# Kernel tuning notes

Measured on AMD Instinct MI355X. Metric: run time of the kernel, lower is better.

The kernel has to match this reference:

```python
import jax, jax.numpy as jnp
import numpy as np

B, N, DIM = 4, 1024, 1024
H, DH = 16, 64
NUM_MEM = 4
TOPK = 64
QK_SCALE = 10.0  # qk_norm_scale


def l2norm(t, eps=1e-12):
    # qk_norm_groups == 1 -> normalize over full head dim
    return t / jnp.clip(jnp.linalg.norm(t, axis=-1, keepdims=True), eps)


def setup_inputs() -> dict:
    key = jax.random.key(0)
    ks = jax.random.split(key, 12)
    s = 0.02
    inp = {
        "x": jax.random.normal(ks[0], (B, N, DIM), dtype=jnp.float32),
        "Wq": jax.random.normal(ks[1], (DIM, H * DH), dtype=jnp.float32) * s,
        "Wk": jax.random.normal(ks[2], (DIM, H * DH), dtype=jnp.float32) * s,
        "Wv": jax.random.normal(ks[3], (DIM, H * DH), dtype=jnp.float32) * s,
        "W_pre_th": jax.random.normal(ks[4], (H, H), dtype=jnp.float32) * (1.0 / H) ** 0.5,
        "W_post_th": jax.random.normal(ks[5], (H, H), dtype=jnp.float32) * (1.0 / H) ** 0.5,
        "mem_k": jax.random.normal(ks[6], (H, NUM_MEM, DH), dtype=jnp.float32),
        "mem_v": jax.random.normal(ks[7], (H, NUM_MEM, DH), dtype=jnp.float32),
        "head_scale_params": jnp.ones((1, H, 1, 1), dtype=jnp.float32),
        "Wg": jax.random.normal(ks[8], (DIM, H * DH), dtype=jnp.float32) * s,
        "bg": jnp.ones((H * DH,), dtype=jnp.float32),
        "Wo": jax.random.normal(ks[9], (H * DH, DIM), dtype=jnp.float32) * s,
    }
    return inp


def reference(x, Wq, Wk, Wv, W_pre_th, W_post_th, mem_k, mem_v,
              head_scale_params, Wg, bg, Wo):
    b, n, _ = x.shape
    # projections -> b h n d
    q = (x @ Wq).reshape(b, n, H, DH).transpose(0, 2, 1, 3)
    k = (x @ Wk).reshape(b, n, H, DH).transpose(0, 2, 1, 3)
    v = (x @ Wv).reshape(b, n, H, DH).transpose(0, 2, 1, 3)

    # memory key/values prepended along the key axis
    mk = jnp.broadcast_to(mem_k[None], (b, H, NUM_MEM, DH))
    mv = jnp.broadcast_to(mem_v[None], (b, H, NUM_MEM, DH))
    k = jnp.concatenate([mk, k], axis=2)
    v = jnp.concatenate([mv, v], axis=2)

    # qk-norm: l2 normalize then fixed scale
    q = l2norm(q)
    k = l2norm(k)

    dots = jnp.einsum("bhid,bhjd->bhij", q, k) * QK_SCALE  # b h n (n+m)
    # pre-softmax talking heads (1x1 conv over head channels)
    dots = jnp.einsum("hg,bgij->bhij", W_pre_th, dots)

    mask_value = -jnp.finfo(dots.dtype).max
    j = n + NUM_MEM
    # causal mask, left-padded False over the memory columns
    col_pos = jnp.arange(j) - NUM_MEM  # mem cols get negative pos -> never masked
    causal = jnp.arange(n)[:, None] < col_pos[None, :]  # (n, j)
    dots = jnp.where(causal[None, None], mask_value, dots)

    # sparse top-k: keep only entries >= k-th largest per row
    top = jax.lax.top_k(dots, TOPK)[0]
    vk = top[..., -1:]
    dots = jnp.where(dots < vk, mask_value, dots)

    attn = jax.nn.softmax(dots, axis=-1)
    # post-softmax talking heads
    attn = jnp.einsum("hg,bgij->bhij", W_post_th, attn)

    out = jnp.einsum("bhij,bhjd->bhid", attn, v)
    out = out * head_scale_params
    out = out.transpose(0, 2, 1, 3).reshape(b, n, H * DH)

    gates = x @ Wg + bg
    out = out * jax.nn.sigmoid(gates)
    return out @ Wo
```

## Files before the change

kernel.cpp:

```cpp
#include <hip/hip_runtime.h>
#include <hip/hip_bf16.h>
#include <float.h>

#define B_ 4
#define N_ 1024
#define H_ 16
#define DH_ 64
#define NM_ 4
#define J_ 1028
#define IT_ 4
#define TOPK_ 64
#define QKSCALE 10.0f
#define KTF_BG 67584
#define VTF_DC 16896

typedef __attribute__((ext_vector_type(8))) short short8;
typedef __attribute__((ext_vector_type(4))) float f32x4;
typedef __attribute__((ext_vector_type(8))) unsigned short ushort8;
typedef __attribute__((ext_vector_type(4))) unsigned int u32x4;
typedef __attribute__((ext_vector_type(2))) unsigned int u32x2;
typedef _Float16 half8 __attribute__((ext_vector_type(8)));

__device__ __forceinline__ unsigned short f2b(float f){
  union { float f; unsigned int i; } c; c.f = f;
  unsigned int r = c.i + 0x7FFFu + ((c.i >> 16) & 1u);
  return (unsigned short)(r >> 16);
}
__device__ __forceinline__ unsigned short f2h(float f){
  return __builtin_bit_cast(unsigned short, (_Float16)f);
}
__device__ __forceinline__ float h2f(unsigned short u){
  return (float)__builtin_bit_cast(_Float16, u);
}
__device__ __forceinline__ unsigned int h2key(unsigned int u){
  return (u & 0x8000u) ? (~u & 0xFFFFu) : (u | 0x8000u);
}
__device__ __forceinline__ float key2f(unsigned int k){
  unsigned int u = (k & 0x8000u) ? (k & 0x7FFFu) : (~k & 0xFFFFu);
  return h2f((unsigned short)u);
}

__global__ __launch_bounds__(256) void k_cvtAll(
    const float* __restrict__ x,  const float* __restrict__ wq,
    const float* __restrict__ wk, const float* __restrict__ wv,
    const float* __restrict__ wg, const float* __restrict__ wo,
    unsigned short* __restrict__ xb, unsigned short* __restrict__ wcatT,
    unsigned short* __restrict__ wobT,
    const float* __restrict__ mk, const float* __restrict__ mv,
    unsigned short* __restrict__ ktF, unsigned short* __restrict__ vtF){
  const int t = threadIdx.x;
  const unsigned bid = blockIdx.x;
  if (bid < 1280){
    __shared__ unsigned short tile[64][70];
    const int which = bid >> 8;
    const int tl = bid & 255;
    const int tr = tl >> 4, tc = tl & 15;
    const float* src = which == 0 ? wq : which == 1 ? wk : which == 2 ? wv : which == 3 ? wg : wo;
    {
      int r = t >> 2, c0 = (t & 3) * 16;
      const float* sp = src + (size_t)(tr * 64 + r) * 1024 + tc * 64 + c0;
      #pragma unroll
      for (int e = 0; e < 16; ++e) tile[r][c0 + e] = f2b(sp[e]);
    }
    __syncthreads();
    {
      int rn = t >> 2, k0 = (t & 3) * 16;
      int n = tc * 64 + rn;
      unsigned short* dp = (which == 4)
        ? wobT + (size_t)n * 1024 + tr * 64 + k0
        : wcatT + ((size_t)which * 1024 + n) * 1024 + tr * 64 + k0;
      ushort8 v0, v1;
      #pragma unroll
      for (int e = 0; e < 8; ++e) v0[e] = tile[k0 + e][rn];
      #pragma unroll
      for (int e = 0; e < 8; ++e) v1[e] = tile[k0 + 8 + e][rn];
      *(ushort8*)dp = v0;
      *(ushort8*)(dp + 8) = v1;
    }
    return;
  }
  if (bid >= 1280 && bid < 1284){
    int h = (bid - 1280) * 4 + (t >> 6);
    int d = t & 63;
    unsigned short kh[4], vh[4];
    #pragma unroll
    for (int mm = 0; mm < 4; ++mm){
      float kv = mk[(h * 4 + mm) * 64 + d];
      float ss = kv * kv;
      #pragma unroll
      for (int off = 32; off; off >>= 1) ss += __shfl_xor(ss, off);
      kh[mm] = f2h(kv / fmaxf(sqrtf(ss), 1e-12f));
      vh[mm] = f2h(mv[(h * 4 + mm) * 64 + d]);
    }
    for (int b = 0; b < B_; ++b){
      int bg = b * 16 + h;
      #pragma unroll
      for (int mm = 0; mm < 4; ++mm)
        ktF[(size_t)bg * KTF_BG + (size_t)(d >> 5) * 512 + (mm + ((d >> 3) & 3) * 16) * 8 + (d & 7)] = kh[mm];
      #pragma unroll
      for (int mm = 0; mm < 4; ++mm)
        vtF[(size_t)bg * KTF_BG + (size_t)(d >> 4) * VTF_DC + (d & 15) * 8 + mm] = vh[mm];
      {
        unsigned int* kz = (unsigned int*)(ktF + (size_t)bg * KTF_BG + 64 * 1024);
        for (int c = d; c < 1024; c += 64) kz[c] = 0u;
      }
      #pragma unroll
      for (int dc = 0; dc < 4; ++dc){
        unsigned int* vz = (unsigned int*)(vtF + (size_t)bg * KTF_BG + (size_t)dc * VTF_DC + 32 * 512);
        for (int c = d; c < 256; c += 64) vz[c] = 0u;
      }
    }
    return;
  }
  int i = (bid - 1284) * 256 + t;
  const int st = (3072 - 1284) * 256;
  for (; i < 4096 * 1024; i += st) xb[i] = f2b(x[i]);
}

__global__ __launch_bounds__(256) void k_gemmF(const unsigned short* __restrict__ A,
                                               const unsigned short* __restrict__ WcT,
                                               unsigned short* __restrict__ qn,
                                               unsigned short* __restrict__ ktF,
                                               unsigned short* __restrict__ vtF,
                                               unsigned short* __restrict__ gate,
                                               const float* __restrict__ bgv)
{
  __shared__ unsigned short As[128][72];
  __shared__ unsigned short Bs[64][72];
  const int t = threadIdx.x;
  const int m0 = blockIdx.y * 128, n0 = blockIdx.x * 64;
  const int l = t & 63, w = t >> 6;
  const int l15 = l & 15, l4 = l >> 4;

  f32x4 acc[2][4];
  #pragma unroll
  for (int a = 0; a < 2; ++a)
    #pragma unroll
    for (int b2 = 0; b2 < 4; ++b2) acc[a][b2] = (f32x4){0.f, 0.f, 0.f, 0.f};

  for (int k0 = 0; k0 < 1024; k0 += 64){
    #pragma unroll
    for (int cc = 0; cc < 4; ++cc){
      int c = t + cc * 256;
      int row = c >> 3, colc = (c & 7) * 8;
      *(ushort8*)&As[row][colc] = *(const ushort8*)&A[(m0 + row) * 1024 + k0 + colc];
    }
    #pragma unroll
    for (int cc = 0; cc < 2; ++cc){
      int c = t + cc * 256;
      int row = c >> 3, colc = (c & 7) * 8;
      *(ushort8*)&Bs[row][colc] = *(const ushort8*)&WcT[(size_t)(n0 + row) * 1024 + k0 + colc];
    }
    __syncthreads();
    #pragma unroll
    for (int ks = 0; ks < 64; ks += 32){
      short8 af[2], bfr[4];
      #pragma unroll
      for (int mf = 0; mf < 2; ++mf) af[mf]  = *(const short8*)&As[w * 32 + mf * 16 + l15][ks + l4 * 8];
      #pragma unroll
      for (int nf = 0; nf < 4; ++nf) bfr[nf] = *(const short8*)&Bs[nf * 16 + l15][ks + l4 * 8];
      #pragma unroll
      for (int mf = 0; mf < 2; ++mf)
        #pragma unroll
        for (int nf = 0; nf < 4; ++nf)
          acc[mf][nf] = __builtin_amdgcn_mfma_f32_16x16x32_bf16(af[mf], bfr[nf], acc[mf][nf], 0, 0, 0);
    }
    __syncthreads();
  }

  const int which = n0 >> 10;
  const int ncol0 = n0 & 1023;
  const int hcol = ncol0 >> 6;
  #pragma unroll
  for (int mf = 0; mf < 2; ++mf){
    if (which == 2){
      int row0 = m0 + w * 32 + mf * 16 + l4 * 4;
      int bb = row0 >> 10;
      int j0 = (row0 & 1023) + NM_;
      int jtE = j0 >> 5, lj = (j0 & 31) >> 3, e0 = j0 & 7;
      #pragma unroll
      for (int nf = 0; nf < 4; ++nf){
        int col = ncol0 + nf * 16 + l15;
        int h = col >> 6, d = col & 63;
        unsigned int lo = (unsigned int)f2h(acc[mf][nf][0]) | ((unsigned int)f2h(acc[mf][nf][1]) << 16);
        unsigned int hi = (unsigned int)f2h(acc[mf][nf][2]) | ((unsigned int)f2h(acc[mf][nf][3]) << 16);
        unsigned short* dst = vtF + (size_t)(bb * 16 + h) * KTF_BG +
                              (size_t)(d >> 4) * VTF_DC + (size_t)jtE * 512 +
                              ((d & 15) + lj * 16) * 8 + e0;
        *(u32x2*)dst = (u32x2){lo, hi};
      }
    } else {
      #pragma unroll
      for (int r = 0; r < 4; ++r){
        int row = m0 + w * 32 + mf * 16 + l4 * 4 + r;
        float rn = 1.f;
        if (which <= 1){
          float ss = 0.f;
          #pragma unroll
          for (int nf = 0; nf < 4; ++nf) ss += acc[mf][nf][r] * acc[mf][nf][r];
          #pragma unroll
          for (int off = 1; off < 16; off <<= 1) ss += __shfl_xor(ss, off);
          rn = 1.f / fmaxf(sqrtf(ss), 1e-12f);
          if (which == 0) rn *= QKSCALE;
        }
        #pragma unroll
        for (int nf = 0; nf < 4; ++nf){
          int col = ncol0 + nf * 16 + l15;
          float v = acc[mf][nf][r];
          int bb = row >> 10, ii = row & 1023;
          if (which == 3){
            float g = v + bgv[3 * 1024 + col];
            gate[(size_t)row * 1024 + col] = f2h(1.f / (1.f + __expf(-g)));
          } else if (which == 0){
            int d = col & 63;
            qn[((size_t)(bb * H_ + hcol) * N_ + ii) * DH_ + d] = f2h(v * rn);
          } else {
            int j = ii + NM_;
            int d = col & 63;
            ktF[(size_t)(bb * 16 + hcol) * KTF_BG + (size_t)(j >> 4) * 1024 +
                (size_t)(d >> 5) * 512 + ((j & 15) + ((d >> 3) & 3) * 16) * 8 + (d & 7)]
              = f2h(v * rn);
          }
        }
      }
    }
  }
}

__global__ __launch_bounds__(256) void k_gemmO(const unsigned short* __restrict__ A,
                                               const unsigned short* __restrict__ WT,
                                               float* __restrict__ outp)
{
  __shared__ unsigned short As[128][72];
  __shared__ unsigned short Bs[64][72];
  const int t = threadIdx.x;
  const int m0 = blockIdx.y * 128, n0 = blockIdx.x * 64;
  const int l = t & 63, w = t >> 6;
  const int l15 = l & 15, l4 = l >> 4;

  f32x4 acc[2][4];
  #pragma unroll
  for (int a = 0; a < 2; ++a)
    #pragma unroll
    for (int b2 = 0; b2 < 4; ++b2) acc[a][b2] = (f32x4){0.f, 0.f, 0.f, 0.f};

  for (int k0 = 0; k0 < 1024; k0 += 64){
    #pragma unroll
    for (int cc = 0; cc < 4; ++cc){
      int c = t + cc * 256;
      int row = c >> 3, colc = (c & 7) * 8;
      *(ushort8*)&As[row][colc] = *(const ushort8*)&A[(m0 + row) * 1024 + k0 + colc];
    }
    #pragma unroll
    for (int cc = 0; cc < 2; ++cc){
      int c = t + cc * 256;
      int row = c >> 3, colc = (c & 7) * 8;
      *(ushort8*)&Bs[row][colc] = *(const ushort8*)&WT[(size_t)(n0 + row) * 1024 + k0 + colc];
    }
    __syncthreads();
    #pragma unroll
    for (int ks = 0; ks < 64; ks += 32){
      short8 af[2], bfr[4];
      #pragma unroll
      for (int mf = 0; mf < 2; ++mf) af[mf]  = *(const short8*)&As[w * 32 + mf * 16 + l15][ks + l4 * 8];
      #pragma unroll
      for (int nf = 0; nf < 4; ++nf) bfr[nf] = *(const short8*)&Bs[nf * 16 + l15][ks + l4 * 8];
      #pragma unroll
      for (int mf = 0; mf < 2; ++mf)
        #pragma unroll
        for (int nf = 0; nf < 4; ++nf)
          acc[mf][nf] = __builtin_amdgcn_mfma_f32_16x16x32_bf16(af[mf], bfr[nf], acc[mf][nf], 0, 0, 0);
    }
    __syncthreads();
  }

  #pragma unroll
  for (int mf = 0; mf < 2; ++mf)
    #pragma unroll
    for (int r = 0; r < 4; ++r){
      int row = m0 + w * 32 + mf * 16 + l4 * 4 + r;
      #pragma unroll
      for (int nf = 0; nf < 4; ++nf)
        outp[(size_t)row * 1024 + n0 + nf * 16 + l15] = acc[mf][nf][r];
    }
}

template<int NJTE_MAX>
__global__ __launch_bounds__(1024) void k_attnM(
  const unsigned short* __restrict__ qn, const unsigned short* __restrict__ ktF,
  const unsigned short* __restrict__ vtF, const float* __restrict__ wpre,
  const float* __restrict__ wpost, const float* __restrict__ hsc,
  const unsigned short* __restrict__ gate, unsigned short* __restrict__ aout,
  int itBase)
{
  constexpr int JSTT = NJTE_MAX * 32 + 8;
  constexpr int NG = (JSTT + 127) / 128;
  __shared__ unsigned short sd[16 * IT_ * JSTT];
  __shared__ unsigned short qls[16 * 4 * 64];
  __shared__ unsigned short wpre16[16 * 32];
  __shared__ unsigned short wpost16[16 * 32];

  const int blk = blockIdx.x;
  const int b = (blk >> 1) & 3;
  const int idx = ((blk >> 3) << 1) | (blk & 1);
  const int it = itBase - idx;
  const int i0 = it * IT_;
  const int nAmax = i0 + IT_ + 4;
  const int nJtA = (nAmax + 15) >> 4;
  const int nJtE = (nAmax + 31) >> 5;
  const int nJtD = nJtE * 2;
  const int jc = nJtE * 32;
  const int t = threadIdx.x;
  const int w = t >> 6, l = t & 63;
  const int l15 = l & 15, l4 = l >> 4;

  if (t < 256){
    int h = t >> 4, g = t & 15;
    wpre16[h * 32 + g]       = f2h(wpre[h * 16 + g]);
    wpre16[h * 32 + 16 + g]  = 0;
    wpost16[h * 32 + g]      = f2h(wpost[h * 16 + g]);
    wpost16[h * 32 + 16 + g] = 0;
  }
  for (int c = t; c < 2048; c += 1024){
    int d2 = c & 31, ii = (c >> 5) & 3, g = c >> 7;
    ((unsigned int*)qls)[c] =
      *(const unsigned int*)(qn + ((size_t)(b * 16 + g) * N_ + i0 + ii) * 64 + d2 * 2);
  }
  __syncthreads();

  {
    const int nw16 = (nJtA > w) ? ((nJtA - w + 15) >> 4) : 0;
    const int ntask = nw16 * 16;
    if (ntask > 0){
      const int tmax = ntask - 1;
      const unsigned short* kl = ktF + (size_t)(b * 16) * KTF_BG + (size_t)l * 8;
      auto kp = [&](int task)->const unsigned short*{
        int tt = task > tmax ? tmax : task;
        int g = tt & 15, jti = tt >> 4;
        return kl + (size_t)g * KTF_BG + (((size_t)(w + jti * 16)) << 10);
      };
      const unsigned short* p0 = kp(0);
      const unsigned short* p1 = kp(1);
      half8 kA0 = *(const half8*)p0, kA1 = *(const half8*)(p0 + 512);
      half8 kB0 = *(const half8*)p1, kB1 = *(const half8*)(p1 + 512);
      for (int task = 0; task < ntask; task += 2){
        half8 cA0 = kA0, cA1 = kA1, cB0 = kB0, cB1 = kB1;
        const unsigned short* pa = kp(task + 2);
        const unsigned short* pb = kp(task + 3);
        kA0 = *(const half8*)pa; kA1 = *(const half8*)(pa + 512);
        kB0 = *(const half8*)pb; kB1 = *(const half8*)(pb + 512);
        #pragma unroll
        for (int s = 0; s < 2; ++s){
          const int tt = task + s;
          const int g = tt & 15, jt = w + ((tt >> 4) << 4);
          const unsigned short* qp = &qls[(g * 4 + (l15 & 3)) * 64 + l4 * 8];
          half8 qf0 = *(const half8*)(qp);
          half8 qf1 = *(const half8*)(qp + 32);
          f32x4 acc = (f32x4){0.f, 0.f, 0.f, 0.f};
          acc = __builtin_amdgcn_mfma_f32_16x16x32_f16(s ? cB0 : cA0, qf0, acc, 0, 0, 0);
          acc = __builtin_amdgcn_mfma_f32_16x16x32_f16(s ? cB1 : cA1, qf1, acc, 0, 0, 0);
          if (l15 < IT_){
            unsigned int pk0 = (unsigned int)f2h(acc[0]) | ((unsigned int)f2h(acc[1]) << 16);
            unsigned int pk1 = (unsigned int)f2h(acc[2]) | ((unsigned int)f2h(acc[3]) << 16);
            unsigned int* dst = (unsigned int*)&sd[(g * IT_ + l15) * JSTT + jt * 16 + l4 * 4];
            dst[0] = pk0; dst[1] = pk1;
          }
        }
      }
    }
  }
  __syncthreads();

  {
    half8 wa = *(const half8*)&wpre16[l15 * 32 + l4 * 8];
    const int ntask = IT_ * nJtA;
    for (int task = w; task < ntask; task += 16){
      const int ii = task & (IT_ - 1), jt = task >> 2;
      unsigned int fb[4] = {0u, 0u, 0u, 0u};
      if (l4 < 2){
        const unsigned short* src = &sd[((l4 * 8) * IT_ + ii) * JSTT + jt * 16 + l15];
        #pragma unroll
        for (int e = 0; e < 8; e += 2){
          unsigned int lo = src[(size_t)(e)     * IT_ * JSTT];
          unsigned int hi = src[(size_t)(e + 1) * IT_ * JSTT];
          fb[e >> 1] = (lo & 0xFFFFu) | (hi << 16);
        }
      }
      f32x4 acc = (f32x4){0.f, 0.f, 0.f, 0.f};
      acc = __builtin_amdgcn_mfma_f32_16x16x32_f16(wa, __builtin_bit_cast(half8, *(u32x4*)fb), acc, 0, 0, 0);
      #pragma unroll
      for (int r = 0; r < 4; ++r)
        sd[((l4 * 4 + r) * IT_ + ii) * JSTT + jt * 16 + l15] = f2h(acc[r]);
    }
  }
  __syncthreads();

  for (int rr = 0; rr < 4; ++rr){
    const int row = w * 4 + rr;
    const int g = row >> 2, ii = row & 3;
    const int nA = i0 + ii + 5;
    unsigned short* rowp = &sd[(g * IT_ + ii) * JSTT];
    unsigned int kw[NG];
    #pragma unroll
    for (int grp = 0; grp < NG; ++grp){
      kw[grp] = 0u;
      if (grp * 128 < jc){
        int j = grp * 128 + l * 2;
        unsigned int u = (j < JSTT) ? *(const unsigned int*)(rowp + j) : 0u;
        unsigned int klo = h2key(u & 0xFFFFu);
        unsigned int khi = h2key(u >> 16);
        if (j     >= nA) klo = 0u;
        if (j + 1 >= nA) khi = 0u;
        kw[grp] = klo | (khi << 16);
      }
    }
    unsigned int kmx = 0u;
    #pragma unroll
    for (int grp = 0; grp < NG; ++grp){
      if (grp * 128 < jc){
        unsigned int m2 = max(kw[grp] >> 16, kw[grp] & 0xFFFFu);
        kmx = max(kmx, m2);
      }
    }
    #pragma unroll
    for (int off = 32; off; off >>= 1) kmx = max(kmx, (unsigned int)__shfl_xor((int)kmx, off));
    const float mx = key2f(kmx);

    unsigned int T = 0u;
    if (nA > TOPK_){
      for (int bit = 15; bit >= 2; --bit){
        unsigned int Tc = T | (1u << bit);
        int c = 0;
        #pragma unroll
        for (int grp = 0; grp < NG; ++grp){
          if (grp * 128 < jc){
            c += __popcll(__ballot((kw[grp] & 0xFFFFu) >= Tc));
            c += __popcll(__ballot((kw[grp] >> 16) >= Tc));
          }
        }
        if (c >= TOPK_){
          T = Tc;
          if (c == TOPK_) break;
        }
      }
    }
    if (T == 0u) T = 1u;

    float s = 0.f;
    float ev[2 * NG];
    #pragma unroll
    for (int grp = 0; grp < NG; ++grp){
      if (grp * 128 < jc){
        unsigned int klo = kw[grp] & 0xFFFFu, khi = kw[grp] >> 16;
        float elo = (klo >= T) ? __expf(key2f(klo) - mx) : 0.f;
        float ehi = (khi >= T) ? __expf(key2f(khi) - mx) : 0.f;
        ev[grp * 2] = elo; ev[grp * 2 + 1] = ehi;
        s += elo + ehi;
      }
    }
    #pragma unroll
    for (int off = 32; off; off >>= 1) s += __shfl_xor(s, off);
    float inv = 1.f / s;
    #pragma unroll
    for (int grp = 0; grp < NG; ++grp){
      if (grp * 128 < jc){
        int j = grp * 128 + l * 2;
        if (j < JSTT)
          *(unsigned int*)(rowp + j) =
            (unsigned int)f2h(ev[grp * 2] * inv) | ((unsigned int)f2h(ev[grp * 2 + 1] * inv) << 16);
      }
    }
  }
  __syncthreads();

  {
    const int ntask = IT_ * nJtD;
    for (int task = w; task < ntask; task += 16){
      const int ii = task & (IT_ - 1), jt = task >> 2;
      half8 wa = *(const half8*)&wpost16[l15 * 32 + l4 * 8];
      unsigned int fb[4] = {0u, 0u, 0u, 0u};
      if (l4 < 2){
        const unsigned short* src = &sd[((l4 * 8) * IT_ + ii) * JSTT + jt * 16 + l15];
        #pragma unroll
        for (int e = 0; e < 8; e += 2){
          unsigned int lo = src[(size_t)(e)     * IT_ * JSTT];
          unsigned int hi = src[(size_t)(e + 1) * IT_ * JSTT];
          fb[e >> 1] = (lo & 0xFFFFu) | (hi << 16);
        }
      }
      f32x4 acc = (f32x4){0.f, 0.f, 0.f, 0.f};
      acc = __builtin_amdgcn_mfma_f32_16x16x32_f16(wa, __builtin_bit_cast(half8, *(u32x4*)fb), acc, 0, 0, 0);
      #pragma unroll
      for (int r = 0; r < 4; ++r)
        sd[((l4 * 4 + r) * IT_ + ii) * JSTT + jt * 16 + l15] = f2h(acc[r]);
    }
  }
  __syncthreads();

  for (int task = w; task < 64; task += 16){
    const int h = task >> 2, dc = task & 3;
    const int bg = b * 16 + h;
    const unsigned short* vbase = vtF + (size_t)bg * KTF_BG + (size_t)dc * VTF_DC + (size_t)l * 8;
    const unsigned short* arow = &sd[(h * IT_ + (l15 & 3)) * JSTT + l4 * 8];
    const int jm = nJtE - 1;
    auto vp_ = [&](int jt)->const half8*{
      int tt = jt > jm ? jm : jt;
      return (const half8*)(vbase + ((size_t)tt << 9));
    };
    half8 vA = *vp_(0), vB = *vp_(1);
    f32x4 acc = (f32x4){0.f, 0.f, 0.f, 0.f};
    int jt = 0;
    for (; jt + 2 <= nJtE; jt += 2){
      half8 cA = vA, cB = vB;
      vA = *vp_(jt + 2); vB = *vp_(jt + 3);
      half8 af0 = *(const half8*)(arow + jt * 32);
      half8 af1 = *(const half8*)(arow + jt * 32 + 32);
      acc = __builtin_amdgcn_mfma_f32_16x16x32_f16(af0, cA, acc, 0, 0, 0);
      acc = __builtin_amdgcn_mfma_f32_16x16x32_f16(af1, cB, acc, 0, 0, 0);
    }
    if (jt < nJtE){
      half8 af0 = *(const half8*)(arow + jt * 32);
      acc = __builtin_amdgcn_mfma_f32_16x16x32_f16(af0, vA, acc, 0, 0, 0);
    }
    if (l4 == 0){
      const float hs = hsc[h];
      #pragma unroll
      for (int r = 0; r < IT_; ++r){
        const int irow = (b << 10) | (i0 + r);
        const size_t o = (size_t)irow * 1024 + h * 64 + dc * 16 + l15;
        aout[o] = f2b(acc[r] * hs * h2f(gate[o]));
      }
    }
  }
}

extern "C" void kernel_launch(void* const* d_in, const int* in_sizes, int n_in,
                              void* d_out, int out_size, void* d_ws, size_t ws_size,
                              hipStream_t stream) {
  const float* x     = (const float*)d_in[0];
  const float* Wq    = (const float*)d_in[1];
  const float* Wk    = (const float*)d_in[2];
  const float* Wv    = (const float*)d_in[3];
  const float* Wpre  = (const float*)d_in[4];
  const float* Wpost = (const float*)d_in[5];
  const float* mk    = (const float*)d_in[6];
  const float* mv    = (const float*)d_in[7];
  const float* hsc   = (const float*)d_in[8];
  const float* Wg    = (const float*)d_in[9];
  const float* bg    = (const float*)d_in[10];
  const float* Wo    = (const float*)d_in[11];
  float* out = (float*)d_out;

  char* ws = (char*)d_ws;
  size_t off = 0;
  auto alloc = [&](size_t bytes) -> void* {
    void* p = ws + off; off += (bytes + 255) & ~(size_t)255; return p;
  };
  unsigned short* xb    = (unsigned short*)alloc((size_t)4096 * 1024 * 2);
  unsigned short* wcatT = (unsigned short*)alloc((size_t)4096 * 1024 * 2);
  unsigned short* wobT  = (unsigned short*)alloc((size_t)1024 * 1024 * 2);
  unsigned short* qn    = (unsigned short*)alloc((size_t)B_ * H_ * N_ * DH_ * 2);
  unsigned short* ktF   = (unsigned short*)alloc((size_t)B_ * H_ * KTF_BG * 2);
  unsigned short* vtF   = (unsigned short*)alloc((size_t)B_ * H_ * KTF_BG * 2);
  unsigned short* gate  = (unsigned short*)alloc((size_t)4096 * 1024 * 2);
  unsigned short* aout  = (unsigned short*)alloc((size_t)4096 * 1024 * 2);

  k_cvtAll<<<3072, 256, 0, stream>>>(x, Wq, Wk, Wv, Wg, Wo, xb, wcatT, wobT,
                                     mk, mv, ktF, vtF);

  k_gemmF<<<dim3(64, 32), 256, 0, stream>>>(xb, wcatT, qn, ktF, vtF, gate, bg - 3 * 1024);

  k_attnM<33><<<512, 1024, 0, stream>>>(qn, ktF, vtF, Wpre, Wpost, hsc, gate, aout, 255);
  k_attnM<17><<<512, 1024, 0, stream>>>(qn, ktF, vtF, Wpre, Wpost, hsc, gate, aout, 127);

  k_gemmO<<<dim3(16, 32), 256, 0, stream>>>(aout, wobT, out);
}
```

Baseline: 318.6 us.

## Fuse pre-softmax talking-heads mix into QK tile loop and set occupancy bounds

Adds a template flag that, for the large-tile attention kernel, applies the pre-softmax talking-heads MFMA per key tile right after that tile's 16 head scores are written. This removes one block-wide barrier and a separate pass over shared memory. It also adds a min-waves argument to launch_bounds for each instantiation to steer register allocation. The fused path relies on each wave owning a key tile and on an LDS waitcnt to order its own writes, which only holds if no other wave touches that tile.

```diff
diff --git a/kernel.cpp b/kernel.cpp
--- a/kernel.cpp
+++ b/kernel.cpp
@@ -285,8 +285,8 @@
     }
 }
 
-template<int NJTE_MAX>
-__global__ __launch_bounds__(1024) void k_attnM(
+template<int NJTE_MAX, int MINW, bool FUSE_AB>
+__global__ __launch_bounds__(1024, MINW) void k_attnM(
   const unsigned short* __restrict__ qn, const unsigned short* __restrict__ ktF,
   const unsigned short* __restrict__ vtF, const float* __restrict__ wpre,
   const float* __restrict__ wpost, const float* __restrict__ hsc,
@@ -329,6 +329,7 @@
   __syncthreads();
 
   {
+    half8 wa = *(const half8*)&wpre16[l15 * 32 + l4 * 8];
     const int nw16 = (nJtA > w) ? ((nJtA - w + 15) >> 4) : 0;
     const int ntask = nw16 * 16;
     if (ntask > 0){
@@ -366,34 +367,57 @@
             dst[0] = pk0; dst[1] = pk1;
           }
         }
-      }
-    }
-  }
-  __syncthreads();
-
-  {
-    half8 wa = *(const half8*)&wpre16[l15 * 32 + l4 * 8];
-    const int ntask = IT_ * nJtA;
-    for (int task = w; task < ntask; task += 16){
-      const int ii = task & (IT_ - 1), jt = task >> 2;
-      unsigned int fb[4] = {0u, 0u, 0u, 0u};
-      if (l4 < 2){
-        const unsigned short* src = &sd[((l4 * 8) * IT_ + ii) * JSTT + jt * 16 + l15];
+        if constexpr (FUSE_AB){
+          if ((task & 15) == 14){
+            const int jt = w + ((task >> 4) << 4);
+            asm volatile("s_waitcnt lgkmcnt(0)" ::: "memory");
+            #pragma unroll
+            for (int ii = 0; ii < IT_; ++ii){
+              unsigned int fb[4] = {0u, 0u, 0u, 0u};
+              if (l4 < 2){
+                const unsigned short* src = &sd[((l4 * 8) * IT_ + ii) * JSTT + jt * 16 + l15];
+                #pragma unroll
+                for (int e = 0; e < 8; e += 2){
+                  unsigned int lo = src[(size_t)(e)     * IT_ * JSTT];
+                  unsigned int hi = src[(size_t)(e + 1) * IT_ * JSTT];
+                  fb[e >> 1] = (lo & 0xFFFFu) | (hi << 16);
+                }
+              }
+              f32x4 pacc = (f32x4){0.f, 0.f, 0.f, 0.f};
+              pacc = __builtin_amdgcn_mfma_f32_16x16x32_f16(wa, __builtin_bit_cast(half8, *(u32x4*)fb), pacc, 0, 0, 0);
+              asm volatile("s_waitcnt lgkmcnt(0)" ::: "memory");
+              #pragma unroll
+              for (int r = 0; r < 4; ++r)
+                sd[((l4 * 4 + r) * IT_ + ii) * JSTT + jt * 16 + l15] = f2h(pacc[r]);
+            }
+          }
+        }
+      }
+    }
+    __syncthreads();
+    if constexpr (!FUSE_AB){
+      const int ntaskB = IT_ * nJtA;
+      for (int task = w; task < ntaskB; task += 16){
+        const int ii = task & (IT_ - 1), jt = task >> 2;
+        unsigned int fb[4] = {0u, 0u, 0u, 0u};
+        if (l4 < 2){
+          const unsigned short* src = &sd[((l4 * 8) * IT_ + ii) * JSTT + jt * 16 + l15];
+          #pragma unroll
+          for (int e = 0; e < 8; e += 2){
+            unsigned int lo = src[(size_t)(e)     * IT_ * JSTT];
+            unsigned int hi = src[(size_t)(e + 1) * IT_ * JSTT];
+            fb[e >> 1] = (lo & 0xFFFFu) | (hi << 16);
+          }
+        }
+        f32x4 acc = (f32x4){0.f, 0.f, 0.f, 0.f};
+        acc = __builtin_amdgcn_mfma_f32_16x16x32_f16(wa, __builtin_bit_cast(half8, *(u32x4*)fb), acc, 0, 0, 0);
         #pragma unroll
-        for (int e = 0; e < 8; e += 2){
-          unsigned int lo = src[(size_t)(e)     * IT_ * JSTT];
-          unsigned int hi = src[(size_t)(e + 1) * IT_ * JSTT];
-          fb[e >> 1] = (lo & 0xFFFFu) | (hi << 16);
-        }
-      }
-      f32x4 acc = (f32x4){0.f, 0.f, 0.f, 0.f};
-      acc = __builtin_amdgcn_mfma_f32_16x16x32_f16(wa, __builtin_bit_cast(half8, *(u32x4*)fb), acc, 0, 0, 0);
-      #pragma unroll
-      for (int r = 0; r < 4; ++r)
-        sd[((l4 * 4 + r) * IT_ + ii) * JSTT + jt * 16 + l15] = f2h(acc[r]);
-    }
-  }
-  __syncthreads();
+        for (int r = 0; r < 4; ++r)
+          sd[((l4 * 4 + r) * IT_ + ii) * JSTT + jt * 16 + l15] = f2h(acc[r]);
+      }
+      __syncthreads();
+    }
+  }
 
   for (int rr = 0; rr < 4; ++rr){
     const int row = w * 4 + rr;
@@ -570,8 +594,8 @@
 
   k_gemmF<<<dim3(64, 32), 256, 0, stream>>>(xb, wcatT, qn, ktF, vtF, gate, bg - 3 * 1024);
 
-  k_attnM<33><<<512, 1024, 0, stream>>>(qn, ktF, vtF, Wpre, Wpost, hsc, gate, aout, 255);
-  k_attnM<17><<<512, 1024, 0, stream>>>(qn, ktF, vtF, Wpre, Wpost, hsc, gate, aout, 127);
+  k_attnM<33, 4, true><<<512, 1024, 0, stream>>>(qn, ktF, vtF, Wpre, Wpost, hsc, gate, aout, 255);
+  k_attnM<17, 8, false><<<512, 1024, 0, stream>>>(qn, ktF, vtF, Wpre, Wpost, hsc, gate, aout, 127);
 
   k_gemmO<<<dim3(16, 32), 256, 0, stream>>>(aout, wobT, out);
 }
```

Result: faster. 312.0 us (-2.1%).
